# Kernel optimization log

Measured on AMD Instinct MI355X. Metric: run time of the kernel, lower is better.

## Reference

```python
import jax, jax.numpy as jnp
import numpy as np

EMB = 1024
HEADS = 16
HEAD_DIM = EMB // HEADS
B, T = 2, 2048
EPS = 1e-5


def setup_inputs() -> dict:
    key = jax.random.key(0)
    ks = jax.random.split(key, 12)
    s_in = (1.0 / np.sqrt(EMB)).astype(np.float32)
    s_hid = (1.0 / np.sqrt(4 * EMB)).astype(np.float32)
    return {
        "x": jax.random.normal(ks[0], (B, T, EMB), jnp.float32),
        "Wq": jax.random.normal(ks[1], (HEADS, EMB, HEAD_DIM), jnp.float32) * s_in,
        "Wk": jax.random.normal(ks[2], (HEADS, EMB, HEAD_DIM), jnp.float32) * s_in,
        "Wv": jax.random.normal(ks[3], (HEADS, EMB, HEAD_DIM), jnp.float32) * s_in,
        "W1": jax.random.normal(ks[4], (EMB, 4 * EMB), jnp.float32) * s_in,
        "b1": jnp.zeros((4 * EMB,), jnp.float32),
        "W2": jax.random.normal(ks[5], (4 * EMB, EMB), jnp.float32) * s_hid,
        "b2": jnp.zeros((EMB,), jnp.float32),
        "g1": jnp.ones((EMB,), jnp.float32),
        "be1": jnp.zeros((EMB,), jnp.float32),
        "g2": jnp.ones((EMB,), jnp.float32),
        "be2": jnp.zeros((EMB,), jnp.float32),
    }


def _layernorm1d(x, gain, bias):
    # Faithful to source: normalize over dim 1 (sequence dim of [B,T,C]),
    # with UNBIASED variance (torch.var default).
    mean = jnp.mean(x, axis=1, keepdims=True)
    var = jnp.var(x, axis=1, keepdims=True, ddof=1)
    return gain * (x - mean) / jnp.sqrt(var + EPS) + bias


def _attention(x, Wq, Wk, Wv):
    Bq, Tq, C = x.shape
    q = jnp.einsum("btc,hcd->bhtd", x, Wq)
    k = jnp.einsum("btc,hcd->bhtd", x, Wk)
    v = jnp.einsum("btc,hcd->bhtd", x, Wv)
    # NOTE: scale uses input channel dim C (=emb_size), as in the source.
    wei = jnp.einsum("bhtd,bhsd->bhts", q, k) * (C ** -0.5)
    causal = jnp.tril(jnp.ones((Tq, Tq), bool))
    wei = jnp.where(causal, wei, -jnp.inf)
    wei = jax.nn.softmax(wei, axis=-1)
    out = jnp.einsum("bhts,bhsd->bhtd", wei, v)
    # concat over heads (dim=-1) == transpose + reshape
    return out.transpose(0, 2, 1, 3).reshape(Bq, Tq, -1)


def reference(x, Wq, Wk, Wv, W1, b1, W2, b2, g1, be1, g2, be2):
    x = x + _attention(_layernorm1d(x, g1, be1), Wq, Wk, Wv)
    h = _layernorm1d(x, g2, be2)
    h = jax.nn.relu(h @ W1 + b1) @ W2 + b2
    return x + h
```

## Files before the change

### kernel.cpp

```cpp
#include <hip/hip_runtime.h>


typedef __bf16 bf16x8 __attribute__((ext_vector_type(8)));
typedef float f32x4 __attribute__((ext_vector_type(4)));
typedef unsigned short u16;
typedef u16 u16x8 __attribute__((ext_vector_type(8)));
typedef u16 u16x4 __attribute__((ext_vector_type(4)));

#define MFMA16 __builtin_amdgcn_mfma_f32_16x16x32_bf16

__device__ __forceinline__ u16 f2bf(float f) {
  return __builtin_bit_cast(u16, (__bf16)f);
}
__device__ __forceinline__ float bf2f(u16 u) {
  return __builtin_bit_cast(float, (unsigned)u << 16);
}
__device__ __forceinline__ bf16x8 ldbf8(const u16* p) {
  return __builtin_bit_cast(bf16x8, *reinterpret_cast<const u16x8*>(p));
}
__device__ __forceinline__ void gll16(const void* g, void* l) {
  __builtin_amdgcn_global_load_lds((const __attribute__((address_space(1))) void*)g,
                                   (__attribute__((address_space(3))) void*)l, 16, 0, 0);
}
template <int N>
__device__ __forceinline__ void wait_vm() {
  if constexpr (N == 0)      asm volatile("s_waitcnt vmcnt(0)" ::: "memory");
  else if constexpr (N == 4) asm volatile("s_waitcnt vmcnt(4)" ::: "memory");
  else if constexpr (N == 8) asm volatile("s_waitcnt vmcnt(8)" ::: "memory");
  else                       asm volatile("s_waitcnt vmcnt(16)" ::: "memory");
}
__device__ __forceinline__ void barrier_raw() {
  asm volatile("" ::: "memory");
  __builtin_amdgcn_s_barrier();
  asm volatile("" ::: "memory");
}

__global__ __launch_bounds__(256) void transpose_big(const float* __restrict__ in,
                                                     u16* __restrict__ out, int K, int N) {
  __shared__ float tile[64][65];
  const int k0 = blockIdx.x * 64, n0 = blockIdx.y * 64;
  const int c = threadIdx.x & 63, rg = threadIdx.x >> 6;
#pragma unroll
  for (int i = 0; i < 16; ++i) {
    int r = rg * 16 + i;
    tile[r][c] = in[(size_t)(k0 + r) * N + n0 + c];
  }
  __syncthreads();
#pragma unroll
  for (int i = 0; i < 16; ++i) {
    int nl = rg * 16 + i;
    out[(size_t)(n0 + nl) * K + k0 + c] = f2bf(tile[c][nl]);
  }
}

__global__ __launch_bounds__(256) void transpose_head(const float* __restrict__ W,
                                                      u16* __restrict__ out, int zoff,
                                                      float scale) {
  __shared__ float tile[64][65];
  const int k0 = blockIdx.x * 64, h = blockIdx.y;
  const float* in = W + (size_t)h * 1024 * 64;
  const int c = threadIdx.x & 63, rg = threadIdx.x >> 6;
#pragma unroll
  for (int i = 0; i < 16; ++i) {
    int r = rg * 16 + i;
    tile[r][c] = in[(size_t)(k0 + r) * 64 + c];
  }
  __syncthreads();
#pragma unroll
  for (int i = 0; i < 16; ++i) {
    int nl = rg * 16 + i;
    out[(size_t)(zoff + h * 64 + nl) * 1024 + k0 + c] = f2bf(tile[c][nl] * scale);
  }
}

__global__ __launch_bounds__(256) void ln_partial(const float* __restrict__ x,
                                                  float2* __restrict__ part) {
  const int b = blockIdx.x >> 4, c0 = (blockIdx.x & 15) * 64;
  const int c = c0 + (threadIdx.x & 63), tg = threadIdx.x >> 6;
  const int t0 = blockIdx.y * 256 + tg * 64;
  float s = 0.f, sq = 0.f;
  const float* p = x + (size_t)(b * 2048 + t0) * 1024 + c;
#pragma unroll 8
  for (int i = 0; i < 64; ++i) {
    float v = p[(size_t)i * 1024];
    s += v; sq += v * v;
  }
  __shared__ float ss[256], sb[256];
  ss[threadIdx.x] = s; sb[threadIdx.x] = sq;
  __syncthreads();
  if (threadIdx.x < 64) {
    s  = ss[threadIdx.x] + ss[threadIdx.x + 64] + ss[threadIdx.x + 128] + ss[threadIdx.x + 192];
    sq = sb[threadIdx.x] + sb[threadIdx.x + 64] + sb[threadIdx.x + 128] + sb[threadIdx.x + 192];
    part[(size_t)(b * 1024 + c) * 8 + blockIdx.y] = make_float2(s, sq);
  }
}

__global__ __launch_bounds__(256) void ln_stats(const float2* __restrict__ part,
                                                float2* __restrict__ stats) {
  const int bc = blockIdx.x * 256 + threadIdx.x;
  float s = 0.f, sq = 0.f;
#pragma unroll
  for (int i = 0; i < 8; ++i) {
    float2 v = part[(size_t)bc * 8 + i];
    s += v.x; sq += v.y;
  }
  const float mean = s * (1.0f / 2048.0f);
  const float var = (sq - 2048.0f * mean * mean) * (1.0f / 2047.0f);
  stats[bc] = make_float2(mean, rsqrtf(var + 1e-5f));
}

__global__ __launch_bounds__(256) void ln_apply(const float* __restrict__ x,
                                                const float2* __restrict__ stats,
                                                const float* __restrict__ g,
                                                const float* __restrict__ be,
                                                u16* __restrict__ out) {
  const size_t flat = ((size_t)blockIdx.x * 256 + threadIdx.x) * 4;
  const int b = (int)(flat >> 21);
  const int c = (int)(flat & 1023);
  float4 xv = *reinterpret_cast<const float4*>(x + flat);
  float vs[4] = {xv.x, xv.y, xv.z, xv.w};
  u16x4 o;
#pragma unroll
  for (int j = 0; j < 4; ++j) {
    float2 st = stats[b * 1024 + c + j];
    o[j] = f2bf(g[c + j] * (vs[j] - st.x) * st.y + be[c + j]);
  }
  *reinterpret_cast<u16x4*>(out + flat) = o;
}

template <int EPI>
__global__ __launch_bounds__(256, 2) void gemm_kernel(const u16* __restrict__ A,
                                                      const u16* __restrict__ Bt,
                                                      u16* __restrict__ outb,
                                                      float* __restrict__ outf,
                                                      const float* __restrict__ bias,
                                                      const float* __restrict__ resid,
                                                      int N, int K) {
  constexpr int BM = 128, BN = 128;
  __shared__ alignas(16) u16 sA[2][BM * 64];
  __shared__ alignas(16) u16 sB[2][BN * 64];
  const int gx = gridDim.x;
  const int nwg = gx * gridDim.y;
  int bid = blockIdx.y * gx + blockIdx.x;
  bid = (bid & 7) * (nwg >> 3) + (bid >> 3);
  const int n0 = (bid % gx) * BN, m0 = (bid / gx) * BM;
  const int tid = threadIdx.x, lane = tid & 63, wid = tid >> 6;
  const int wm = (wid >> 1) * 64, wn = (wid & 1) * 64;
  const int lr = lane & 15, lg = lane >> 4;
  const int srow = lane >> 3;
  const int sgr = (lane & 7) ^ srow;
  const int x7 = lr & 7;
  f32x4 acc[4][4] = {};

  auto stage = [&](int buf, int k0) {
#pragma unroll
    for (int i = 0; i < 8; ++i) {
      const int c = wid * 8 + i;
      if (c < 16) {
        const int r = c * 8 + srow;
        gll16(A + (size_t)(m0 + r) * K + k0 + sgr * 8, &sA[buf][c * 512]);
      } else {
        const int r = (c - 16) * 8 + srow;
        gll16(Bt + (size_t)(n0 + r) * K + k0 + sgr * 8, &sB[buf][(c - 16) * 512]);
      }
    }
  };

  const int nsteps = K >> 6;
  stage(0, 0);
  int cur = 0;
  for (int t = 0; t < nsteps; ++t) {
    if (t + 1 < nsteps) {
      stage(cur ^ 1, (t + 1) * 64);
      wait_vm<8>();
    } else {
      wait_vm<0>();
    }
    barrier_raw();
    bf16x8 af[4][2], bfr[4][2];
#pragma unroll
    for (int mi = 0; mi < 4; ++mi)
#pragma unroll
      for (int kk = 0; kk < 2; ++kk)
        af[mi][kk] = ldbf8(&sA[cur][(wm + mi * 16 + lr) * 64 + (((kk * 4 + lg) ^ x7) * 8)]);
#pragma unroll
    for (int ni = 0; ni < 4; ++ni)
#pragma unroll
      for (int kk = 0; kk < 2; ++kk)
        bfr[ni][kk] = ldbf8(&sB[cur][(wn + ni * 16 + lr) * 64 + (((kk * 4 + lg) ^ x7) * 8)]);
#pragma unroll
    for (int kk = 0; kk < 2; ++kk)
#pragma unroll
      for (int mi = 0; mi < 4; ++mi)
#pragma unroll
        for (int ni = 0; ni < 4; ++ni)
          acc[mi][ni] = MFMA16(af[mi][kk], bfr[ni][kk], acc[mi][ni], 0, 0, 0);
    barrier_raw();
    cur ^= 1;
  }

#pragma unroll
  for (int mi = 0; mi < 4; ++mi)
#pragma unroll
    for (int ni = 0; ni < 4; ++ni)
#pragma unroll
      for (int r = 0; r < 4; ++r) {
        const int row = m0 + wm + mi * 16 + lg * 4 + r;
        const int col = n0 + wn + ni * 16 + lr;
        float v = acc[mi][ni][r];
        if (EPI == 0) {
          outb[(size_t)row * N + col] = f2bf(v);
        } else if (EPI == 1) {
          v += bias[col];
          v = fmaxf(v, 0.f);
          outb[(size_t)row * N + col] = f2bf(v);
        } else {
          v += bias[col] + resid[(size_t)row * N + col];
          outf[(size_t)row * N + col] = v;
        }
      }
}

__global__ __launch_bounds__(256) void attn_partial(const u16* __restrict__ qk,
                                                    const u16* __restrict__ vt,
                                                    u16* __restrict__ Opart,
                                                    float2* __restrict__ ml) {
  const int xr = 79 - (int)blockIdx.x;
  int qb, ch, nc;
  if (xr < 8)       { qb = xr;                ch = 0;            nc = 1; }
  else if (xr < 24) { qb = 8 + ((xr - 8) >> 1);  ch = (xr - 8) & 1;  nc = 2; }
  else if (xr < 48) { qb = 16 + (xr - 24) / 3;   ch = (xr - 24) % 3; nc = 3; }
  else              { qb = 24 + ((xr - 48) >> 2); ch = (xr - 48) & 3; nc = 4; }
  const int nt_tot = qb + 1;
  const int t0 = (ch * nt_tot) / nc;
  const int t1 = ((ch + 1) * nt_tot) / nc;
  const int bh = blockIdx.y, b = bh >> 4, h = bh & 15;
  const int slot = bh * 80 + xr;
  const int q0 = qb * 64;
  const int tid = threadIdx.x, lane = tid & 63, w = tid >> 6;
  const int lr = lane & 15, lg = lane >> 4;
  __shared__ alignas(16) u16 sK[2][64 * 64];
  __shared__ alignas(16) u16 sV[2][64 * 64];
  __shared__ alignas(16) u16 sP[4][16 * 64];

  const size_t qrow = (size_t)(b * 2048 + q0 + w * 16 + lr) * 2048 + h * 64;
  const bf16x8 aq0 = ldbf8(qk + qrow + lg * 8);
  const bf16x8 aq1 = ldbf8(qk + qrow + 32 + lg * 8);

  float m_i[4], l_i[4];
  f32x4 acc[4];
#pragma unroll
  for (int r = 0; r < 4; ++r) { m_i[r] = -1e30f; l_i[r] = 0.f; }
#pragma unroll
  for (int dn = 0; dn < 4; ++dn) acc[dn] = f32x4{0.f, 0.f, 0.f, 0.f};

  auto stage = [&](int buf, int s0) {
#pragma unroll
    for (int i = 0; i < 2; ++i) {
      const int c = w * 2 + i;
      const int g = c * 64 + lane;
      const int row = g >> 3;
      const int cs = (g & 7) ^ (row & 7);
      gll16(qk + (size_t)(b * 2048 + s0 + row) * 2048 + 1024 + h * 64 + cs * 8,
            &sK[buf][c * 512]);
      gll16(vt + (size_t)(h * 64 + row) * 4096 + b * 2048 + s0 + cs * 8,
            &sV[buf][c * 512]);
    }
  };

  stage(0, t0 * 64);

  for (int t = t0; t < t1; ++t) {
    const int buf = (t - t0) & 1;
    if (t + 1 < t1) {
      stage(buf ^ 1, (t + 1) * 64);
      wait_vm<4>();
    } else {
      wait_vm<0>();
    }
    barrier_raw();

    const u16* Kb = sK[buf];
    const u16* Vb = sV[buf];
    f32x4 sf[4];
    __builtin_amdgcn_s_setprio(1);
#pragma unroll
    for (int sn = 0; sn < 4; ++sn) {
      const int row = sn * 16 + lr;
      const int x7 = lr & 7;
      bf16x8 k0f = ldbf8(&Kb[row * 64 + ((lg ^ x7) * 8)]);
      bf16x8 k1f = ldbf8(&Kb[row * 64 + (((4 + lg) ^ x7) * 8)]);
      f32x4 z = {0.f, 0.f, 0.f, 0.f};
      z = MFMA16(aq0, k0f, z, 0, 0, 0);
      z = MFMA16(aq1, k1f, z, 0, 0, 0);
      sf[sn] = z;
    }
    __builtin_amdgcn_s_setprio(0);

    if (t == nt_tot - 1) {
      const int qlb = w * 16 + lg * 4;
#pragma unroll
      for (int sn = 0; sn < 4; ++sn)
#pragma unroll
        for (int r = 0; r < 4; ++r)
          if (sn * 16 + lr > qlb + r) sf[sn][r] = -1e30f;
    }

    float pm[4];
    bool need = false;
#pragma unroll
    for (int r = 0; r < 4; ++r) {
      pm[r] = fmaxf(fmaxf(sf[0][r], sf[1][r]), fmaxf(sf[2][r], sf[3][r]));
      need = need || (pm[r] > m_i[r] + 8.f);
    }
    if (__any(need)) {
#pragma unroll
      for (int r = 0; r < 4; ++r) {
        float mx = pm[r];
        mx = fmaxf(mx, __shfl_xor(mx, 1, 16));
        mx = fmaxf(mx, __shfl_xor(mx, 2, 16));
        mx = fmaxf(mx, __shfl_xor(mx, 4, 16));
        mx = fmaxf(mx, __shfl_xor(mx, 8, 16));
        const float mnew = fmaxf(m_i[r], mx);
        const float al = exp2f(m_i[r] - mnew);
        l_i[r] *= al;
        acc[0][r] *= al; acc[1][r] *= al; acc[2][r] *= al; acc[3][r] *= al;
        m_i[r] = mnew;
      }
    }

    const int x7p = lr & 7;
#pragma unroll
    for (int r = 0; r < 4; ++r) {
      const float p0 = exp2f(sf[0][r] - m_i[r]), p1 = exp2f(sf[1][r] - m_i[r]);
      const float p2 = exp2f(sf[2][r] - m_i[r]), p3 = exp2f(sf[3][r] - m_i[r]);
      l_i[r] += (p0 + p1) + (p2 + p3);
      const int prow = lg * 4 + r;
      const int pb = prow * 64, px = prow & 7;
      sP[w][pb + (((lr >> 3) ^ px) * 8) + (lr & 7)]       = f2bf(p0);
      sP[w][pb + (((2 + (lr >> 3)) ^ px) * 8) + (lr & 7)] = f2bf(p1);
      sP[w][pb + (((4 + (lr >> 3)) ^ px) * 8) + (lr & 7)] = f2bf(p2);
      sP[w][pb + (((6 + (lr >> 3)) ^ px) * 8) + (lr & 7)] = f2bf(p3);
    }

    const bf16x8 pa0 = ldbf8(&sP[w][lr * 64 + ((lg ^ x7p) * 8)]);
    const bf16x8 pa1 = ldbf8(&sP[w][lr * 64 + (((4 + lg) ^ x7p) * 8)]);
    __builtin_amdgcn_s_setprio(1);
#pragma unroll
    for (int dn = 0; dn < 4; ++dn) {
      const int row = dn * 16 + lr;
      bf16x8 v0f = ldbf8(&Vb[row * 64 + ((lg ^ x7p) * 8)]);
      bf16x8 v1f = ldbf8(&Vb[row * 64 + (((4 + lg) ^ x7p) * 8)]);
      acc[dn] = MFMA16(pa0, v0f, acc[dn], 0, 0, 0);
      acc[dn] = MFMA16(pa1, v1f, acc[dn], 0, 0, 0);
    }
    __builtin_amdgcn_s_setprio(0);
    barrier_raw();
  }

  const int rbase = w * 16 + lg * 4;
#pragma unroll
  for (int r = 0; r < 4; ++r) {
    float ls = l_i[r];
    ls += __shfl_xor(ls, 1, 16);
    ls += __shfl_xor(ls, 2, 16);
    ls += __shfl_xor(ls, 4, 16);
    ls += __shfl_xor(ls, 8, 16);
    const int row = rbase + r;
    if (lr == 0) ml[(size_t)slot * 64 + row] = make_float2(m_i[r], ls);
#pragma unroll
    for (int dn = 0; dn < 4; ++dn)
      Opart[((size_t)slot * 64 + row) * 64 + dn * 16 + lr] = f2bf(acc[dn][r]);
  }
}

__global__ __launch_bounds__(256) void attn_merge(const u16* __restrict__ Opart,
                                                  const float2* __restrict__ ml,
                                                  const float* __restrict__ x,
                                                  float* __restrict__ x2) {
  const int qb = blockIdx.x, bh = blockIdx.y, b = bh >> 4, h = bh & 15;
  int nc, s0;
  if (qb < 8)       { nc = 1; s0 = qb; }
  else if (qb < 16) { nc = 2; s0 = 8 + (qb - 8) * 2; }
  else if (qb < 24) { nc = 3; s0 = 24 + (qb - 16) * 3; }
  else              { nc = 4; s0 = 48 + (qb - 24) * 4; }
  const size_t slot0 = (size_t)bh * 80 + s0;
  const int tid = threadIdx.x;
  const int row = tid >> 2, d0 = (tid & 3) * 16;

  float wgt[4];
  float mmax = -1e30f, lsum = 0.f;
  for (int i = 0; i < nc; ++i) {
    float2 v = ml[(slot0 + i) * 64 + row];
    wgt[i] = v.x;
    mmax = fmaxf(mmax, v.x);
  }
  for (int i = 0; i < nc; ++i) {
    float2 v = ml[(slot0 + i) * 64 + row];
    wgt[i] = exp2f(wgt[i] - mmax);
    lsum += wgt[i] * v.y;
  }
  const float inv = 1.0f / lsum;

#pragma unroll
  for (int half = 0; half < 2; ++half) {
    const int d = d0 + half * 8;
    float o[8] = {0.f, 0.f, 0.f, 0.f, 0.f, 0.f, 0.f, 0.f};
    for (int i = 0; i < nc; ++i) {
      u16x8 v = *reinterpret_cast<const u16x8*>(&Opart[((slot0 + i) * 64 + row) * 64 + d]);
#pragma unroll
      for (int j = 0; j < 8; ++j) o[j] += wgt[i] * bf2f(v[j]);
    }
    const size_t idx = ((size_t)(b * 2048 + qb * 64 + row)) * 1024 + h * 64 + d;
    float4 x0 = *reinterpret_cast<const float4*>(x + idx);
    float4 x1 = *reinterpret_cast<const float4*>(x + idx + 4);
    float4 o0 = make_float4(x0.x + o[0] * inv, x0.y + o[1] * inv, x0.z + o[2] * inv, x0.w + o[3] * inv);
    float4 o1 = make_float4(x1.x + o[4] * inv, x1.y + o[5] * inv, x1.z + o[6] * inv, x1.w + o[7] * inv);
    *reinterpret_cast<float4*>(x2 + idx) = o0;
    *reinterpret_cast<float4*>(x2 + idx + 4) = o1;
  }
}

extern "C" void kernel_launch(void* const* d_in, const int* in_sizes, int n_in,
                              void* d_out, int out_size, void* d_ws, size_t ws_size,
                              hipStream_t stream) {
  const float* x   = (const float*)d_in[0];
  const float* Wq  = (const float*)d_in[1];
  const float* Wk  = (const float*)d_in[2];
  const float* Wv  = (const float*)d_in[3];
  const float* W1  = (const float*)d_in[4];
  const float* b1  = (const float*)d_in[5];
  const float* W2  = (const float*)d_in[6];
  const float* b2  = (const float*)d_in[7];
  const float* g1  = (const float*)d_in[8];
  const float* be1 = (const float*)d_in[9];
  const float* g2  = (const float*)d_in[10];
  const float* be2 = (const float*)d_in[11];
  float* out = (float*)d_out;

  char* ws = (char*)d_ws;
  size_t off = 0;
  auto alloc = [&](size_t bytes) { char* p = ws + off; off += (bytes + 255) & ~(size_t)255; return p; };
  u16*    qkb   = (u16*)alloc(4096ull * 2048 * 2);
  u16*    vtb   = (u16*)alloc(1024ull * 4096 * 2);
  (void)alloc(4096ull * 1024 * 2);
  u16*    h1    = qkb;
  float*  x2    = (float*)alloc(4096ull * 1024 * 4);
  u16*    hbuf  = (u16*)alloc(4096ull * 1024 * 2);
  u16*    wqkvt = (u16*)alloc(3072ull * 1024 * 2);
  u16*    w1t   = (u16*)alloc(4096ull * 1024 * 2);
  u16*    w2t   = (u16*)alloc(1024ull * 4096 * 2);
  float2* part  = (float2*)alloc(2048ull * 8 * 8);
  float2* stats = (float2*)alloc(2048ull * 8);
  u16*    Opart = (u16*)alloc(32ull * 80 * 64 * 64 * 2);
  float2* ml    = (float2*)alloc(32ull * 80 * 64 * 8);
  (void)ws_size; (void)in_sizes; (void)n_in; (void)out_size;

  const float SC = 0.03125f * 1.44269504088896341f;
  transpose_head<<<dim3(16, 16), 256, 0, stream>>>(Wq, wqkvt, 0, SC);
  transpose_head<<<dim3(16, 16), 256, 0, stream>>>(Wk, wqkvt, 1024, 1.0f);
  transpose_head<<<dim3(16, 16), 256, 0, stream>>>(Wv, wqkvt, 2048, 1.0f);
  transpose_big<<<dim3(16, 64), 256, 0, stream>>>(W1, w1t, 1024, 4096);
  transpose_big<<<dim3(64, 16), 256, 0, stream>>>(W2, w2t, 4096, 1024);

  ln_partial<<<dim3(32, 8), 256, 0, stream>>>(x, part);
  ln_stats<<<8, 256, 0, stream>>>(part, stats);
  ln_apply<<<4096, 256, 0, stream>>>(x, stats, g1, be1, hbuf);

  gemm_kernel<0><<<dim3(16, 32), 256, 0, stream>>>(hbuf, wqkvt, qkb, nullptr, nullptr, nullptr, 2048, 1024);
  gemm_kernel<0><<<dim3(32, 8), 256, 0, stream>>>(wqkvt + 2048 * 1024, hbuf, vtb, nullptr, nullptr, nullptr, 4096, 1024);

  attn_partial<<<dim3(80, 32), 256, 0, stream>>>(qkb, vtb, Opart, ml);
  attn_merge<<<dim3(32, 32), 256, 0, stream>>>(Opart, ml, x, x2);

  ln_partial<<<dim3(32, 8), 256, 0, stream>>>(x2, part);
  ln_stats<<<8, 256, 0, stream>>>(part, stats);
  ln_apply<<<4096, 256, 0, stream>>>(x2, stats, g2, be2, hbuf);

  gemm_kernel<1><<<dim3(32, 32), 256, 0, stream>>>(hbuf, w1t, h1, nullptr, b1, nullptr, 4096, 1024);

  gemm_kernel<2><<<dim3(8, 32), 256, 0, stream>>>(h1, w2t, nullptr, out, b2, x2, 1024, 4096);
}
```

Measured before the change: 255.0 us.

## Restructure attention to share K/V tiles across query-block pairs and narrow small GEMM tiles

Result: slower. 268.7 us (+5.4%).

```diff
diff --git a/kernel.cpp b/kernel.cpp
--- a/kernel.cpp
+++ b/kernel.cpp
@@ -25,7 +25,8 @@
 template <int N>
 __device__ __forceinline__ void wait_vm() {
   if constexpr (N == 0)      asm volatile("s_waitcnt vmcnt(0)" ::: "memory");
-  else if constexpr (N == 4) asm volatile("s_waitcnt vmcnt(4)" ::: "memory");
+  else if constexpr (N == 2) asm volatile("s_waitcnt vmcnt(2)" ::: "memory");
+  else if constexpr (N == 6) asm volatile("s_waitcnt vmcnt(6)" ::: "memory");
   else if constexpr (N == 8) asm volatile("s_waitcnt vmcnt(8)" ::: "memory");
   else                       asm volatile("s_waitcnt vmcnt(16)" ::: "memory");
 }
@@ -33,6 +34,12 @@
   asm volatile("" ::: "memory");
   __builtin_amdgcn_s_barrier();
   asm volatile("" ::: "memory");
+}
+__device__ __forceinline__ int qb_off(int qb) {
+  if (qb < 8)  return qb;
+  if (qb < 16) return 8 + (qb - 8) * 2;
+  if (qb < 24) return 24 + (qb - 16) * 3;
+  return 48 + (qb - 24) * 4;
 }
 
 __global__ __launch_bounds__(256) void transpose_big(const float* __restrict__ in,
@@ -53,10 +60,14 @@
   }
 }
 
-__global__ __launch_bounds__(256) void transpose_head(const float* __restrict__ W,
-                                                      u16* __restrict__ out, int zoff,
-                                                      float scale) {
+__global__ __launch_bounds__(256) void transpose_head3(const float* __restrict__ Wq,
+                                                       const float* __restrict__ Wk,
+                                                       const float* __restrict__ Wv,
+                                                       u16* __restrict__ out, float scale) {
   __shared__ float tile[64][65];
+  const int z = blockIdx.z;
+  const float* W = z == 0 ? Wq : (z == 1 ? Wk : Wv);
+  const float sc = z == 0 ? scale : 1.0f;
   const int k0 = blockIdx.x * 64, h = blockIdx.y;
   const float* in = W + (size_t)h * 1024 * 64;
   const int c = threadIdx.x & 63, rg = threadIdx.x >> 6;
@@ -69,7 +80,7 @@
 #pragma unroll
   for (int i = 0; i < 16; ++i) {
     int nl = rg * 16 + i;
-    out[(size_t)(zoff + h * 64 + nl) * 1024 + k0 + c] = f2bf(tile[c][nl] * scale);
+    out[(size_t)(z * 1024 + h * 64 + nl) * 1024 + k0 + c] = f2bf(tile[c][nl] * sc);
   }
 }
 
@@ -128,15 +139,18 @@
   *reinterpret_cast<u16x4*>(out + flat) = o;
 }
 
-template <int EPI>
-__global__ __launch_bounds__(256, 2) void gemm_kernel(const u16* __restrict__ A,
-                                                      const u16* __restrict__ Bt,
-                                                      u16* __restrict__ outb,
-                                                      float* __restrict__ outf,
-                                                      const float* __restrict__ bias,
-                                                      const float* __restrict__ resid,
-                                                      int N, int K) {
-  constexpr int BM = 128, BN = 128;
+template <int WTN, int EPI, int MINW>
+__global__ __launch_bounds__(256, MINW) void gemm_kernel(const u16* __restrict__ A,
+                                                         const u16* __restrict__ Bt,
+                                                         u16* __restrict__ outb,
+                                                         float* __restrict__ outf,
+                                                         const float* __restrict__ bias,
+                                                         const float* __restrict__ resid,
+                                                         int N, int K) {
+  constexpr int BM = 128, BN = 2 * WTN;
+  constexpr int NI = WTN / 16;
+  constexpr int BCH = BN / 8;
+  constexpr int LPW = (16 + BCH) / 4;
   __shared__ alignas(16) u16 sA[2][BM * 64];
   __shared__ alignas(16) u16 sB[2][BN * 64];
   const int gx = gridDim.x;
@@ -145,17 +159,17 @@
   bid = (bid & 7) * (nwg >> 3) + (bid >> 3);
   const int n0 = (bid % gx) * BN, m0 = (bid / gx) * BM;
   const int tid = threadIdx.x, lane = tid & 63, wid = tid >> 6;
-  const int wm = (wid >> 1) * 64, wn = (wid & 1) * 64;
+  const int wm = (wid >> 1) * 64, wn = (wid & 1) * WTN;
   const int lr = lane & 15, lg = lane >> 4;
   const int srow = lane >> 3;
   const int sgr = (lane & 7) ^ srow;
   const int x7 = lr & 7;
-  f32x4 acc[4][4] = {};
+  f32x4 acc[4][NI] = {};
 
   auto stage = [&](int buf, int k0) {
 #pragma unroll
-    for (int i = 0; i < 8; ++i) {
-      const int c = wid * 8 + i;
+    for (int i = 0; i < LPW; ++i) {
+      const int c = wid * LPW + i;
       if (c < 16) {
         const int r = c * 8 + srow;
         gll16(A + (size_t)(m0 + r) * K + k0 + sgr * 8, &sA[buf][c * 512]);
@@ -172,19 +186,19 @@
   for (int t = 0; t < nsteps; ++t) {
     if (t + 1 < nsteps) {
       stage(cur ^ 1, (t + 1) * 64);
-      wait_vm<8>();
+      wait_vm<LPW>();
     } else {
       wait_vm<0>();
     }
     barrier_raw();
-    bf16x8 af[4][2], bfr[4][2];
+    bf16x8 af[4][2], bfr[NI][2];
 #pragma unroll
     for (int mi = 0; mi < 4; ++mi)
 #pragma unroll
       for (int kk = 0; kk < 2; ++kk)
         af[mi][kk] = ldbf8(&sA[cur][(wm + mi * 16 + lr) * 64 + (((kk * 4 + lg) ^ x7) * 8)]);
 #pragma unroll
-    for (int ni = 0; ni < 4; ++ni)
+    for (int ni = 0; ni < NI; ++ni)
 #pragma unroll
       for (int kk = 0; kk < 2; ++kk)
         bfr[ni][kk] = ldbf8(&sB[cur][(wn + ni * 16 + lr) * 64 + (((kk * 4 + lg) ^ x7) * 8)]);
@@ -193,7 +207,7 @@
 #pragma unroll
       for (int mi = 0; mi < 4; ++mi)
 #pragma unroll
-        for (int ni = 0; ni < 4; ++ni)
+        for (int ni = 0; ni < NI; ++ni)
           acc[mi][ni] = MFMA16(af[mi][kk], bfr[ni][kk], acc[mi][ni], 0, 0, 0);
     barrier_raw();
     cur ^= 1;
@@ -202,7 +216,7 @@
 #pragma unroll
   for (int mi = 0; mi < 4; ++mi)
 #pragma unroll
-    for (int ni = 0; ni < 4; ++ni)
+    for (int ni = 0; ni < NI; ++ni)
 #pragma unroll
       for (int r = 0; r < 4; ++r) {
         const int row = m0 + wm + mi * 16 + lg * 4 + r;
@@ -221,29 +235,30 @@
       }
 }
 
-__global__ __launch_bounds__(256) void attn_partial(const u16* __restrict__ qk,
-                                                    const u16* __restrict__ vt,
-                                                    u16* __restrict__ Opart,
-                                                    float2* __restrict__ ml) {
-  const int xr = 79 - (int)blockIdx.x;
-  int qb, ch, nc;
-  if (xr < 8)       { qb = xr;                ch = 0;            nc = 1; }
-  else if (xr < 24) { qb = 8 + ((xr - 8) >> 1);  ch = (xr - 8) & 1;  nc = 2; }
-  else if (xr < 48) { qb = 16 + (xr - 24) / 3;   ch = (xr - 24) % 3; nc = 3; }
-  else              { qb = 24 + ((xr - 48) >> 2); ch = (xr - 48) & 3; nc = 4; }
-  const int nt_tot = qb + 1;
-  const int t0 = (ch * nt_tot) / nc;
-  const int t1 = ((ch + 1) * nt_tot) / nc;
+__global__ __launch_bounds__(512, 6) void attn_partial(const u16* __restrict__ qk,
+                                                       const u16* __restrict__ vt,
+                                                       u16* __restrict__ Opart,
+                                                       float2* __restrict__ ml) {
+  const int xr = 39 - (int)blockIdx.x;
+  int j, i;
+  if (xr < 16)      { j = 0; i = xr; }
+  else if (xr < 28) { j = 1; i = xr - 16; }
+  else if (xr < 36) { j = 2; i = xr - 28; }
+  else              { j = 3; i = xr - 36; }
+  const int qb1 = j * 8 + 2 * i;
   const int bh = blockIdx.y, b = bh >> 4, h = bh & 15;
-  const int slot = bh * 80 + xr;
-  const int q0 = qb * 64;
   const int tid = threadIdx.x, lane = tid & 63, w = tid >> 6;
+  const int qsel = w >> 2, wl = w & 3;
+  const int qb = qb1 + qsel;
   const int lr = lane & 15, lg = lane >> 4;
+  const int t_lo = 8 * j;
+  const int t_hi_raw = 8 * (j + 1);
+  const int t_hi = (qb1 + 2 < t_hi_raw) ? qb1 + 2 : t_hi_raw;
   __shared__ alignas(16) u16 sK[2][64 * 64];
   __shared__ alignas(16) u16 sV[2][64 * 64];
-  __shared__ alignas(16) u16 sP[4][16 * 64];
-
-  const size_t qrow = (size_t)(b * 2048 + q0 + w * 16 + lr) * 2048 + h * 64;
+  __shared__ alignas(16) u16 sP[8][16 * 64];
+
+  const size_t qrow = (size_t)(b * 2048 + qb * 64 + wl * 16 + lr) * 2048 + h * 64;
   const bf16x8 aq0 = ldbf8(qk + qrow + lg * 8);
   const bf16x8 aq1 = ldbf8(qk + qrow + 32 + lg * 8);
 
@@ -255,110 +270,109 @@
   for (int dn = 0; dn < 4; ++dn) acc[dn] = f32x4{0.f, 0.f, 0.f, 0.f};
 
   auto stage = [&](int buf, int s0) {
-#pragma unroll
-    for (int i = 0; i < 2; ++i) {
-      const int c = w * 2 + i;
-      const int g = c * 64 + lane;
-      const int row = g >> 3;
-      const int cs = (g & 7) ^ (row & 7);
-      gll16(qk + (size_t)(b * 2048 + s0 + row) * 2048 + 1024 + h * 64 + cs * 8,
-            &sK[buf][c * 512]);
-      gll16(vt + (size_t)(h * 64 + row) * 4096 + b * 2048 + s0 + cs * 8,
-            &sV[buf][c * 512]);
-    }
+    const int g = w * 64 + lane;
+    const int row = g >> 3;
+    const int cs = (g & 7) ^ (row & 7);
+    gll16(qk + (size_t)(b * 2048 + s0 + row) * 2048 + 1024 + h * 64 + cs * 8,
+          &sK[buf][w * 512]);
+    gll16(vt + (size_t)(h * 64 + row) * 4096 + b * 2048 + s0 + cs * 8,
+          &sV[buf][w * 512]);
   };
 
-  stage(0, t0 * 64);
-
-  for (int t = t0; t < t1; ++t) {
-    const int buf = (t - t0) & 1;
-    if (t + 1 < t1) {
+  stage(0, t_lo * 64);
+
+  for (int t = t_lo; t < t_hi; ++t) {
+    const int buf = (t - t_lo) & 1;
+    if (t + 1 < t_hi) {
       stage(buf ^ 1, (t + 1) * 64);
-      wait_vm<4>();
+      wait_vm<2>();
     } else {
       wait_vm<0>();
     }
     barrier_raw();
 
-    const u16* Kb = sK[buf];
-    const u16* Vb = sV[buf];
-    f32x4 sf[4];
-    __builtin_amdgcn_s_setprio(1);
-#pragma unroll
-    for (int sn = 0; sn < 4; ++sn) {
-      const int row = sn * 16 + lr;
-      const int x7 = lr & 7;
-      bf16x8 k0f = ldbf8(&Kb[row * 64 + ((lg ^ x7) * 8)]);
-      bf16x8 k1f = ldbf8(&Kb[row * 64 + (((4 + lg) ^ x7) * 8)]);
-      f32x4 z = {0.f, 0.f, 0.f, 0.f};
-      z = MFMA16(aq0, k0f, z, 0, 0, 0);
-      z = MFMA16(aq1, k1f, z, 0, 0, 0);
-      sf[sn] = z;
+    if (t <= qb) {
+      const u16* Kb = sK[buf];
+      const u16* Vb = sV[buf];
+      f32x4 sf[4];
+      __builtin_amdgcn_s_setprio(1);
+#pragma unroll
+      for (int sn = 0; sn < 4; ++sn) {
+        const int row = sn * 16 + lr;
+        const int x7 = lr & 7;
+        bf16x8 k0f = ldbf8(&Kb[row * 64 + ((lg ^ x7) * 8)]);
+        bf16x8 k1f = ldbf8(&Kb[row * 64 + (((4 + lg) ^ x7) * 8)]);
+        f32x4 z = {0.f, 0.f, 0.f, 0.f};
+        z = MFMA16(aq0, k0f, z, 0, 0, 0);
+        z = MFMA16(aq1, k1f, z, 0, 0, 0);
+        sf[sn] = z;
+      }
+      __builtin_amdgcn_s_setprio(0);
+
+      if (t == qb) {
+        const int qlb = wl * 16 + lg * 4;
+#pragma unroll
+        for (int sn = 0; sn < 4; ++sn)
+#pragma unroll
+          for (int r = 0; r < 4; ++r)
+            if (sn * 16 + lr > qlb + r) sf[sn][r] = -1e30f;
+      }
+
+      float pm[4];
+      bool need = false;
+#pragma unroll
+      for (int r = 0; r < 4; ++r) {
+        pm[r] = fmaxf(fmaxf(sf[0][r], sf[1][r]), fmaxf(sf[2][r], sf[3][r]));
+        need = need || (pm[r] > m_i[r] + 8.f);
+      }
+      if (__any(need)) {
+#pragma unroll
+        for (int r = 0; r < 4; ++r) {
+          float mx = pm[r];
+          mx = fmaxf(mx, __shfl_xor(mx, 1, 16));
+          mx = fmaxf(mx, __shfl_xor(mx, 2, 16));
+          mx = fmaxf(mx, __shfl_xor(mx, 4, 16));
+          mx = fmaxf(mx, __shfl_xor(mx, 8, 16));
+          const float mnew = fmaxf(m_i[r], mx);
+          const float al = exp2f(m_i[r] - mnew);
+          l_i[r] *= al;
+          acc[0][r] *= al; acc[1][r] *= al; acc[2][r] *= al; acc[3][r] *= al;
+          m_i[r] = mnew;
+        }
+      }
+
+      const int x7p = lr & 7;
+#pragma unroll
+      for (int r = 0; r < 4; ++r) {
+        const float p0 = exp2f(sf[0][r] - m_i[r]), p1 = exp2f(sf[1][r] - m_i[r]);
+        const float p2 = exp2f(sf[2][r] - m_i[r]), p3 = exp2f(sf[3][r] - m_i[r]);
+        l_i[r] += (p0 + p1) + (p2 + p3);
+        const int prow = lg * 4 + r;
+        const int pb = prow * 64, px = prow & 7;
+        sP[w][pb + (((lr >> 3) ^ px) * 8) + (lr & 7)]       = f2bf(p0);
+        sP[w][pb + (((2 + (lr >> 3)) ^ px) * 8) + (lr & 7)] = f2bf(p1);
+        sP[w][pb + (((4 + (lr >> 3)) ^ px) * 8) + (lr & 7)] = f2bf(p2);
+        sP[w][pb + (((6 + (lr >> 3)) ^ px) * 8) + (lr & 7)] = f2bf(p3);
+      }
+
+      const bf16x8 pa0 = ldbf8(&sP[w][lr * 64 + ((lg ^ x7p) * 8)]);
+      const bf16x8 pa1 = ldbf8(&sP[w][lr * 64 + (((4 + lg) ^ x7p) * 8)]);
+      __builtin_amdgcn_s_setprio(1);
+#pragma unroll
+      for (int dn = 0; dn < 4; ++dn) {
+        const int row = dn * 16 + lr;
+        bf16x8 v0f = ldbf8(&Vb[row * 64 + ((lg ^ x7p) * 8)]);
+        bf16x8 v1f = ldbf8(&Vb[row * 64 + (((4 + lg) ^ x7p) * 8)]);
+        acc[dn] = MFMA16(pa0, v0f, acc[dn], 0, 0, 0);
+        acc[dn] = MFMA16(pa1, v1f, acc[dn], 0, 0, 0);
+      }
+      __builtin_amdgcn_s_setprio(0);
     }
-    __builtin_amdgcn_s_setprio(0);
-
-    if (t == nt_tot - 1) {
-      const int qlb = w * 16 + lg * 4;
-#pragma unroll
-      for (int sn = 0; sn < 4; ++sn)
-#pragma unroll
-        for (int r = 0; r < 4; ++r)
-          if (sn * 16 + lr > qlb + r) sf[sn][r] = -1e30f;
-    }
-
-    float pm[4];
-    bool need = false;
-#pragma unroll
-    for (int r = 0; r < 4; ++r) {
-      pm[r] = fmaxf(fmaxf(sf[0][r], sf[1][r]), fmaxf(sf[2][r], sf[3][r]));
-      need = need || (pm[r] > m_i[r] + 8.f);
-    }
-    if (__any(need)) {
-#pragma unroll
-      for (int r = 0; r < 4; ++r) {
-        float mx = pm[r];
-        mx = fmaxf(mx, __shfl_xor(mx, 1, 16));
-        mx = fmaxf(mx, __shfl_xor(mx, 2, 16));
-        mx = fmaxf(mx, __shfl_xor(mx, 4, 16));
-        mx = fmaxf(mx, __shfl_xor(mx, 8, 16));
-        const float mnew = fmaxf(m_i[r], mx);
-        const float al = exp2f(m_i[r] - mnew);
-        l_i[r] *= al;
-        acc[0][r] *= al; acc[1][r] *= al; acc[2][r] *= al; acc[3][r] *= al;
-        m_i[r] = mnew;
-      }
-    }
-
-    const int x7p = lr & 7;
-#pragma unroll
-    for (int r = 0; r < 4; ++r) {
-      const float p0 = exp2f(sf[0][r] - m_i[r]), p1 = exp2f(sf[1][r] - m_i[r]);
-      const float p2 = exp2f(sf[2][r] - m_i[r]), p3 = exp2f(sf[3][r] - m_i[r]);
-      l_i[r] += (p0 + p1) + (p2 + p3);
-      const int prow = lg * 4 + r;
-      const int pb = prow * 64, px = prow & 7;
-      sP[w][pb + (((lr >> 3) ^ px) * 8) + (lr & 7)]       = f2bf(p0);
-      sP[w][pb + (((2 + (lr >> 3)) ^ px) * 8) + (lr & 7)] = f2bf(p1);
-      sP[w][pb + (((4 + (lr >> 3)) ^ px) * 8) + (lr & 7)] = f2bf(p2);
-      sP[w][pb + (((6 + (lr >> 3)) ^ px) * 8) + (lr & 7)] = f2bf(p3);
-    }
-
-    const bf16x8 pa0 = ldbf8(&sP[w][lr * 64 + ((lg ^ x7p) * 8)]);
-    const bf16x8 pa1 = ldbf8(&sP[w][lr * 64 + (((4 + lg) ^ x7p) * 8)]);
-    __builtin_amdgcn_s_setprio(1);
-#pragma unroll
-    for (int dn = 0; dn < 4; ++dn) {
-      const int row = dn * 16 + lr;
-      bf16x8 v0f = ldbf8(&Vb[row * 64 + ((lg ^ x7p) * 8)]);
-      bf16x8 v1f = ldbf8(&Vb[row * 64 + (((4 + lg) ^ x7p) * 8)]);
-      acc[dn] = MFMA16(pa0, v0f, acc[dn], 0, 0, 0);
-      acc[dn] = MFMA16(pa1, v1f, acc[dn], 0, 0, 0);
-    }
-    __builtin_amdgcn_s_setprio(0);
     barrier_raw();
   }
 
-  const int rbase = w * 16 + lg * 4;
+  const int slot = bh * 80 + qb_off(qb) + j;
+  const int rbase = wl * 16 + lg * 4;
 #pragma unroll
   for (int r = 0; r < 4; ++r) {
     float ls = l_i[r];
@@ -379,12 +393,8 @@
                                                   const float* __restrict__ x,
                                                   float* __restrict__ x2) {
   const int qb = blockIdx.x, bh = blockIdx.y, b = bh >> 4, h = bh & 15;
-  int nc, s0;
-  if (qb < 8)       { nc = 1; s0 = qb; }
-  else if (qb < 16) { nc = 2; s0 = 8 + (qb - 8) * 2; }
-  else if (qb < 24) { nc = 3; s0 = 24 + (qb - 16) * 3; }
-  else              { nc = 4; s0 = 48 + (qb - 24) * 4; }
-  const size_t slot0 = (size_t)bh * 80 + s0;
+  const int nc = (qb >> 3) + 1;
+  const size_t slot0 = (size_t)bh * 80 + qb_off(qb);
   const int tid = threadIdx.x;
   const int row = tid >> 2, d0 = (tid & 3) * 16;
 
@@ -409,7 +419,7 @@
     for (int i = 0; i < nc; ++i) {
       u16x8 v = *reinterpret_cast<const u16x8*>(&Opart[((slot0 + i) * 64 + row) * 64 + d]);
 #pragma unroll
-      for (int j = 0; j < 8; ++j) o[j] += wgt[i] * bf2f(v[j]);
+      for (int jj = 0; jj < 8; ++jj) o[jj] += wgt[i] * bf2f(v[jj]);
     }
     const size_t idx = ((size_t)(b * 2048 + qb * 64 + row)) * 1024 + h * 64 + d;
     float4 x0 = *reinterpret_cast<const float4*>(x + idx);
@@ -457,9 +467,7 @@
   (void)ws_size; (void)in_sizes; (void)n_in; (void)out_size;
 
   const float SC = 0.03125f * 1.44269504088896341f;
-  transpose_head<<<dim3(16, 16), 256, 0, stream>>>(Wq, wqkvt, 0, SC);
-  transpose_head<<<dim3(16, 16), 256, 0, stream>>>(Wk, wqkvt, 1024, 1.0f);
-  transpose_head<<<dim3(16, 16), 256, 0, stream>>>(Wv, wqkvt, 2048, 1.0f);
+  transpose_head3<<<dim3(16, 16, 3), 256, 0, stream>>>(Wq, Wk, Wv, wqkvt, SC);
   transpose_big<<<dim3(16, 64), 256, 0, stream>>>(W1, w1t, 1024, 4096);
   transpose_big<<<dim3(64, 16), 256, 0, stream>>>(W2, w2t, 4096, 1024);
 
@@ -467,17 +475,17 @@
   ln_stats<<<8, 256, 0, stream>>>(part, stats);
   ln_apply<<<4096, 256, 0, stream>>>(x, stats, g1, be1, hbuf);
 
-  gemm_kernel<0><<<dim3(16, 32), 256, 0, stream>>>(hbuf, wqkvt, qkb, nullptr, nullptr, nullptr, 2048, 1024);
-  gemm_kernel<0><<<dim3(32, 8), 256, 0, stream>>>(wqkvt + 2048 * 1024, hbuf, vtb, nullptr, nullptr, nullptr, 4096, 1024);
-
-  attn_partial<<<dim3(80, 32), 256, 0, stream>>>(qkb, vtb, Opart, ml);
+  gemm_kernel<64, 0, 2><<<dim3(16, 32), 256, 0, stream>>>(hbuf, wqkvt, qkb, nullptr, nullptr, nullptr, 2048, 1024);
+  gemm_kernel<32, 0, 3><<<dim3(64, 8), 256, 0, stream>>>(wqkvt + 2048 * 1024, hbuf, vtb, nullptr, nullptr, nullptr, 4096, 1024);
+
+  attn_partial<<<dim3(40, 32), 512, 0, stream>>>(qkb, vtb, Opart, ml);
   attn_merge<<<dim3(32, 32), 256, 0, stream>>>(Opart, ml, x, x2);
 
   ln_partial<<<dim3(32, 8), 256, 0, stream>>>(x2, part);
   ln_stats<<<8, 256, 0, stream>>>(part, stats);
   ln_apply<<<4096, 256, 0, stream>>>(x2, stats, g2, be2, hbuf);
 
-  gemm_kernel<1><<<dim3(32, 32), 256, 0, stream>>>(hbuf, w1t, h1, nullptr, b1, nullptr, 4096, 1024);
-
-  gemm_kernel<2><<<dim3(8, 32), 256, 0, stream>>>(h1, w2t, nullptr, out, b2, x2, 1024, 4096);
-}
+  gemm_kernel<64, 1, 2><<<dim3(32, 32), 256, 0, stream>>>(hbuf, w1t, h1, nullptr, b1, nullptr, 4096, 1024);
+
+  gemm_kernel<32, 2, 3><<<dim3(16, 32), 256, 0, stream>>>(h1, w2t, nullptr, out, b2, x2, 1024, 4096);
+}
```
